# Performance work log

Measured on AMD Instinct MI355X. Metric: run time of the kernel, lower is better.

The kernel has to match this reference:

```python
import jax, jax.numpy as jnp
import numpy as np

S = 8          # num_slots
DSLOT = 128    # slot_dim
D_IN = 768     # input feature dim
ITERS = 3      # slot_att_iter
RES = 21       # 336 // 16
NGRID = RES * RES   # 441 grid positions
NTOK = 441          # tokens kept per frame (no drop here)
NFRAME = 2
F_ = 2 * NFRAME + 1  # 5 frames per clip
CLIPS = 8
B = CLIPS * F_       # 40
SIGMA = 5.0
SCALE = DSLOT ** -0.5
EPS = 1e-8


def layernorm(x, g, b):
    m = x.mean(-1, keepdims=True)
    v = ((x - m) ** 2).mean(-1, keepdims=True)
    return (x - m) * jax.lax.rsqrt(v + 1e-5) * g + b


def setup_inputs() -> dict:
    key = jax.random.key(0)
    ks = iter(jax.random.split(key, 64))
    def nrm(shape, s=0.02):
        return jax.random.normal(next(ks), shape, jnp.float32) * s
    xs = jnp.linspace(-1.0, 1.0, RES)
    ys = jnp.linspace(-1.0, 1.0, RES)
    gx, gy = jnp.meshgrid(xs, ys)  # indexing='xy' as in torch
    abs_grid = jnp.stack([gx.ravel(), gy.ravel()], axis=-1)  # [NGRID, 2]
    return {
        "inputs": jax.random.normal(next(ks), (B, NTOK, D_IN), jnp.float32),
        "token_indices": jnp.sort(jax.random.randint(next(ks), (B, NTOK), 0, NGRID), axis=-1),
        "abs_grid": abs_grid,
        "slots_init": nrm((1, S, DSLOT), 0.1),
        "S_p_init": nrm((1, S, 1, 2), 0.02),
        "S_s_init": jax.random.uniform(next(ks), (1, S, 1, 2), jnp.float32, 0.3, 0.7),
        "WQ": nrm((DSLOT, DSLOT)), "ln_g": jnp.ones((DSLOT,)), "ln_b": jnp.zeros((DSLOT,)),
        "gru_w_ih": nrm((DSLOT, 3 * DSLOT)), "gru_w_hh": nrm((DSLOT, 3 * DSLOT)),
        "gru_b_ih": jnp.zeros((3 * DSLOT,)), "gru_b_hh": jnp.zeros((3 * DSLOT,)),
        "mlp_ln_g": jnp.ones((DSLOT,)), "mlp_ln_b": jnp.zeros((DSLOT,)),
        "mlp_w1": nrm((DSLOT, 4 * DSLOT)), "mlp_b1": jnp.zeros((4 * DSLOT,)),
        "mlp_w2": nrm((4 * DSLOT, DSLOT)), "mlp_b2": jnp.zeros((DSLOT,)),
        "WK": nrm((DSLOT, DSLOT)), "WV": nrm((DSLOT, DSLOT)),
        "Wg": nrm((2, DSLOT)), "bg": jnp.zeros((DSLOT,)),
        "Wf1": nrm((DSLOT, DSLOT)), "bf1": jnp.zeros((DSLOT,)),
        "Wf2": nrm((DSLOT, DSLOT)), "bf2": jnp.zeros((DSLOT,)),
        "im_ln1_g": jnp.ones((D_IN,)), "im_ln1_b": jnp.zeros((D_IN,)),
        "im_w1": nrm((D_IN, D_IN)), "im_b1": jnp.zeros((D_IN,)),
        "im_w2": nrm((D_IN, DSLOT)), "im_b2": jnp.zeros((DSLOT,)),
        "im_ln2_g": jnp.ones((DSLOT,)), "im_ln2_b": jnp.zeros((DSLOT,)),
        "fin_w": nrm((DSLOT, DSLOT)), "fin_b": jnp.zeros((DSLOT,)),
    }


def _forward(inputs, token_indices, abs_grid, slots_init, S_p_init, S_s_init,
             WQ, ln_g, ln_b, gru_w_ih, gru_w_hh, gru_b_ih, gru_b_hh,
             mlp_ln_g, mlp_ln_b, mlp_w1, mlp_b1, mlp_w2, mlp_b2,
             WK, WV, Wg, bg, Wf1, bf1, Wf2, bf2,
             im_ln1_g, im_ln1_b, im_w1, im_b1, im_w2, im_b2, im_ln2_g, im_ln2_b,
             fin_w, fin_b):
    Bb = inputs.shape[0]
    # initial_mlp: LN -> Linear -> ReLU -> Linear -> LN
    x = layernorm(inputs, im_ln1_g, im_ln1_b)
    x = jax.nn.relu(x @ im_w1 + im_b1)
    x = x @ im_w2 + im_b2
    x = layernorm(x, im_ln2_g, im_ln2_b)          # [B, N, Dslot]
    # K/V projections of inputs are slot-independent; compute once.
    Kx = x @ WK                                    # [B, N, Dslot]
    Vx = x @ WV
    ag = abs_grid[token_indices]                   # [B, N, 2] per-batch gather
    slots = jnp.broadcast_to(slots_init, (Bb, S, DSLOT))
    S_p = jnp.broadcast_to(S_p_init, (Bb, S, 1, 2))
    S_s = jnp.broadcast_to(S_s_init, (Bb, S, 1, 2))

    def f_net(z):  # f = Linear -> ReLU -> Linear
        return jax.nn.relu(z @ Wf1 + bf1) @ Wf2 + bf2

    attn = None
    for t in range(ITERS + 1):
        slots_prev = slots
        sn = layernorm(slots, ln_g, ln_b)
        rel = (ag[:, None] - S_p) / (S_s * SIGMA)  # [B, S, N, 2]
        gr = rel @ Wg + bg                          # [B, S, N, Dslot]
        k = f_net(Kx[:, None] + gr)
        v = f_net(Vx[:, None] + gr)
        q = sn @ WQ                                 # [B, S, Dslot]
        dots = jnp.einsum('bsd,bsjd->bsj', q, k) * SCALE
        attn = jax.nn.softmax(dots, axis=1) + EPS   # softmax over slots
        attn = attn / attn.sum(-1, keepdims=True)   # renormalize over tokens
        updates = jnp.einsum('bsjd,bsj->bsd', v, attn)
        S_p = jnp.einsum('bjd,bsj->bsd', ag, attn)[:, :, None, :]
        S_s = jnp.sqrt(jnp.einsum('bsjd,bsj->bsd', (ag[:, None] - S_p) ** 2, attn))[:, :, None, :]
        if t != ITERS:
            # torch GRUCell
            xg = updates.reshape(-1, DSLOT)
            hg = slots_prev.reshape(-1, DSLOT)
            gi = xg @ gru_w_ih + gru_b_ih
            gh = hg @ gru_w_hh + gru_b_hh
            i_r, i_z, i_n = jnp.split(gi, 3, axis=-1)
            h_r, h_z, h_n = jnp.split(gh, 3, axis=-1)
            r = jax.nn.sigmoid(i_r + h_r)
            z = jax.nn.sigmoid(i_z + h_z)
            n = jnp.tanh(i_n + r * h_n)
            slots = ((1.0 - z) * n + z * hg).reshape(Bb, S, DSLOT)
            # residual pre-LN MLP (dropout is identity in eval)
            y = layernorm(slots, mlp_ln_g, mlp_ln_b)
            y = jax.nn.relu(y @ mlp_w1 + mlp_b1) @ mlp_w2 + mlp_b2
            slots = slots + y
    slots = slots @ fin_w + fin_b
    attn_out = attn.reshape(-1, F_, S, NTOK)[:, NFRAME]  # center frame
    return slots, attn_out


def reference(inputs, token_indices, abs_grid, slots_init, S_p_init, S_s_init,
              WQ, ln_g, ln_b, gru_w_ih, gru_w_hh, gru_b_ih, gru_b_hh,
              mlp_ln_g, mlp_ln_b, mlp_w1, mlp_b1, mlp_w2, mlp_b2,
              WK, WV, Wg, bg, Wf1, bf1, Wf2, bf2,
              im_ln1_g, im_ln1_b, im_w1, im_b1, im_w2, im_b2, im_ln2_g, im_ln2_b,
              fin_w, fin_b):
    return _forward(inputs, token_indices, abs_grid, slots_init, S_p_init, S_s_init,
                    WQ, ln_g, ln_b, gru_w_ih, gru_w_hh, gru_b_ih, gru_b_hh,
                    mlp_ln_g, mlp_ln_b, mlp_w1, mlp_b1, mlp_w2, mlp_b2,
                    WK, WV, Wg, bg, Wf1, bf1, Wf2, bf2,
                    im_ln1_g, im_ln1_b, im_w1, im_b1, im_w2, im_b2, im_ln2_g, im_ln2_b,
                    fin_w, fin_b)
```

## Files before the change

### kernel.cpp

```cpp
#include <hip/hip_runtime.h>
#include <cstdio>

#define NB 40
#define NS 8
#define NT 441
#define DIN 768
#define DD 128
#define NTOT (NB*NT)
#define FSCALE 0.08838834764831843f

typedef short s8v __attribute__((ext_vector_type(8)));
typedef float f4v __attribute__((ext_vector_type(4)));

__device__ inline ushort f2bf(float f){
  unsigned u = __float_as_uint(f);
  unsigned r = (u + 0x7fffu + ((u >> 16) & 1u)) >> 16;
  return (ushort)r;
}
__device__ inline float bf2f(ushort h){ return __uint_as_float(((unsigned)h) << 16); }

struct PP {
  const float *inputs; const int *tok_idx; const float *abs_grid;
  const float *slots_init, *Sp_init, *Ss_init;
  const float *WQ, *ln_g, *ln_b;
  const float *gru_w_ih, *gru_w_hh, *gru_b_ih, *gru_b_hh;
  const float *mlp_ln_g, *mlp_ln_b, *mlp_w1, *mlp_b1, *mlp_w2, *mlp_b2;
  const float *WK, *WV, *Wg, *bg, *Wf1, *bf1, *Wf2, *bf2;
  const float *im_ln1_g, *im_ln1_b, *im_w1, *im_b1, *im_w2, *im_b2, *im_ln2_g, *im_ln2_b;
  const float *fin_w, *fin_b;
  float *x, *A_K, *A_V, *ag, *WKf, *WVf, *Wg1, *c1, *Wf2T;
  float *slots, *Sp0, *Sp1, *Ss0, *Ss1, *qW, *qb, *dots, *attn;
  float *hbar_part, *Sp_part, *hbar;
  ushort *xnh, *xnl, *hh, *hl, *W1Th, *W1Tl, *W2Th, *W2Tl;
  float *out;
};

__global__ __launch_bounds__(128) void prep_weights(PP p){
  int r = blockIdx.x, d = threadIdx.x;
  float accK = 0.f, accV = 0.f;
  for (int kk = 0; kk < DD; kk++){
    float w = p.Wf1[kk*DD + d];
    accK = fmaf(p.WK[r*DD+kk], w, accK);
    accV = fmaf(p.WV[r*DD+kk], w, accV);
  }
  p.WKf[r*DD+d] = accK; p.WVf[r*DD+d] = accV;
  if (r < 2){
    float a = 0.f;
    for (int kk = 0; kk < DD; kk++) a = fmaf(p.Wg[r*DD+kk], p.Wf1[kk*DD+d], a);
    p.Wg1[r*DD+d] = a;
  }
  if (r == 2){
    float a = 0.f;
    for (int kk = 0; kk < DD; kk++) a = fmaf(p.bg[kk], p.Wf1[kk*DD+d], a);
    p.c1[d] = a + p.bf1[d];
  }
  p.Wf2T[d*DD + r] = p.Wf2[r*DD + d];
}

__global__ __launch_bounds__(256) void transpose_split(const float* __restrict__ W,
                                                       ushort* __restrict__ WTh,
                                                       ushort* __restrict__ WTl,
                                                       int K, int N){
  __shared__ float tile[64][65];
  int tid = threadIdx.x;
  int k0 = blockIdx.x * 64, n0 = blockIdx.y * 64;
  #pragma unroll
  for (int i = 0; i < 4; i++){
    int k = i*16 + (tid >> 4);
    int n4 = (tid & 15) * 4;
    float4 v = *(const float4*)(W + (long)(k0+k)*N + n0 + n4);
    tile[k][n4+0] = v.x; tile[k][n4+1] = v.y; tile[k][n4+2] = v.z; tile[k][n4+3] = v.w;
  }
  __syncthreads();
  #pragma unroll
  for (int i = 0; i < 4; i++){
    int n = i*16 + (tid >> 4);
    int k4 = (tid & 15) * 4;
    ushort4 h4, l4;
    float v0 = tile[k4+0][n], v1 = tile[k4+1][n], v2 = tile[k4+2][n], v3 = tile[k4+3][n];
    h4.x = f2bf(v0); l4.x = f2bf(v0 - bf2f(h4.x));
    h4.y = f2bf(v1); l4.y = f2bf(v1 - bf2f(h4.y));
    h4.z = f2bf(v2); l4.z = f2bf(v2 - bf2f(h4.z));
    h4.w = f2bf(v3); l4.w = f2bf(v3 - bf2f(h4.w));
    *(ushort4*)(WTh + (long)(n0+n)*K + k0 + k4) = h4;
    *(ushort4*)(WTl + (long)(n0+n)*K + k0 + k4) = l4;
  }
}

__global__ __launch_bounds__(256) void ln1_split(PP p){
  int tok = blockIdx.x*4 + (threadIdx.x >> 6);
  int l = threadIdx.x & 63;
  const float* src = p.inputs + (long)tok*DIN;
  float4 v[3];
  float s = 0.f, s2 = 0.f;
  #pragma unroll
  for (int pp = 0; pp < 3; pp++){
    v[pp] = *(const float4*)(src + pp*256 + l*4);
    s  += v[pp].x + v[pp].y + v[pp].z + v[pp].w;
    s2 += v[pp].x*v[pp].x + v[pp].y*v[pp].y + v[pp].z*v[pp].z + v[pp].w*v[pp].w;
  }
  #pragma unroll
  for (int m = 1; m < 64; m <<= 1){ s += __shfl_xor(s, m); s2 += __shfl_xor(s2, m); }
  float mean = s*(1.f/DIN), var = s2*(1.f/DIN) - mean*mean;
  float rstd = rsqrtf(var + 1e-5f);
  #pragma unroll
  for (int pp = 0; pp < 3; pp++){
    int idx = pp*256 + l*4;
    float4 g = *(const float4*)(p.im_ln1_g + idx);
    float4 b = *(const float4*)(p.im_ln1_b + idx);
    float y0 = (v[pp].x-mean)*rstd*g.x + b.x;
    float y1 = (v[pp].y-mean)*rstd*g.y + b.y;
    float y2 = (v[pp].z-mean)*rstd*g.z + b.z;
    float y3 = (v[pp].w-mean)*rstd*g.w + b.w;
    ushort4 h4, l4;
    h4.x = f2bf(y0); l4.x = f2bf(y0 - bf2f(h4.x));
    h4.y = f2bf(y1); l4.y = f2bf(y1 - bf2f(h4.y));
    h4.z = f2bf(y2); l4.z = f2bf(y2 - bf2f(h4.z));
    h4.w = f2bf(y3); l4.w = f2bf(y3 - bf2f(h4.w));
    *(ushort4*)(p.xnh + (long)tok*DIN + idx) = h4;
    *(ushort4*)(p.xnl + (long)tok*DIN + idx) = l4;
  }
}

template<int EPI>
__global__ __launch_bounds__(256) void gemm_split(
    const ushort* __restrict__ Ah, const ushort* __restrict__ Al,
    const ushort* __restrict__ Bh, const ushort* __restrict__ Bl,
    const float* __restrict__ bias,
    ushort* __restrict__ Ch, ushort* __restrict__ Cl,
    float* __restrict__ Xout, const float* __restrict__ g2, const float* __restrict__ b2,
    int M)
{
  __shared__ __align__(16) char smem[64*132*4];
  ushort* As = (ushort*)smem;
  ushort* Bs = (ushort*)(smem + 10240);
  int tid = threadIdx.x;
  int n0 = blockIdx.x * 128, m0 = blockIdx.y * 64;
  int w = tid >> 6, lane = tid & 63;
  f4v acc[4][2];
  #pragma unroll
  for (int mf = 0; mf < 4; mf++)
    #pragma unroll
    for (int nf = 0; nf < 2; nf++) acc[mf][nf] = (f4v)(0.f);

  for (int kb = 0; kb < DIN; kb += 32){
    __syncthreads();
    #pragma unroll
    for (int i = 0; i < 2; i++){
      int c = tid + i*256;
      int s = c >> 8, r = (c >> 2) & 63, kg = c & 3;
      int gr = min(m0 + r, M-1);
      const float4 va = *(const float4*)((s ? Al : Ah) + (long)gr*DIN + kb + kg*8);
      *(float4*)(As + s*2560 + r*40 + kg*8) = va;
    }
    #pragma unroll
    for (int i = 0; i < 4; i++){
      int c = tid + i*256;
      int s = c >> 9, r = (c >> 2) & 127, kg = c & 3;
      const float4 vb = *(const float4*)((s ? Bl : Bh) + (long)(n0 + r)*DIN + kb + kg*8);
      *(float4*)(Bs + s*5120 + r*40 + kg*8) = vb;
    }
    __syncthreads();
    int kg = lane >> 4, rA = lane & 15;
    s8v a0[4], a1[4], b0[2], b1[2];
    #pragma unroll
    for (int mf = 0; mf < 4; mf++){
      a0[mf] = *(const s8v*)(As +        (mf*16 + rA)*40 + kg*8);
      a1[mf] = *(const s8v*)(As + 2560 + (mf*16 + rA)*40 + kg*8);
    }
    #pragma unroll
    for (int nf = 0; nf < 2; nf++){
      int rb = w*32 + nf*16 + rA;
      b0[nf] = *(const s8v*)(Bs +        rb*40 + kg*8);
      b1[nf] = *(const s8v*)(Bs + 5120 + rb*40 + kg*8);
    }
    #pragma unroll
    for (int mf = 0; mf < 4; mf++)
      #pragma unroll
      for (int nf = 0; nf < 2; nf++){
        acc[mf][nf] = __builtin_amdgcn_mfma_f32_16x16x32_bf16(a0[mf], b0[nf], acc[mf][nf], 0, 0, 0);
        acc[mf][nf] = __builtin_amdgcn_mfma_f32_16x16x32_bf16(a0[mf], b1[nf], acc[mf][nf], 0, 0, 0);
        acc[mf][nf] = __builtin_amdgcn_mfma_f32_16x16x32_bf16(a1[mf], b0[nf], acc[mf][nf], 0, 0, 0);
      }
  }

  int rbase = (lane >> 4) * 4, cn = lane & 15;
  if (EPI == 1){
    #pragma unroll
    for (int mf = 0; mf < 4; mf++)
      #pragma unroll
      for (int nf = 0; nf < 2; nf++){
        int n = n0 + w*32 + nf*16 + cn;
        float bs = bias[n];
        #pragma unroll
        for (int r = 0; r < 4; r++){
          int m = m0 + mf*16 + rbase + r;
          if (m < M){
            float v = fmaxf(acc[mf][nf][r] + bs, 0.f);
            ushort h = f2bf(v);
            Ch[(long)m*DIN + n] = h;
            Cl[(long)m*DIN + n] = f2bf(v - bf2f(h));
          }
        }
      }
  } else {
    __syncthreads();
    float* Dl = (float*)smem;
    #pragma unroll
    for (int mf = 0; mf < 4; mf++)
      #pragma unroll
      for (int nf = 0; nf < 2; nf++){
        int n = w*32 + nf*16 + cn;
        float bs = bias[n];
        #pragma unroll
        for (int r = 0; r < 4; r++)
          Dl[(mf*16 + rbase + r)*132 + n] = acc[mf][nf][r] + bs;
      }
    __syncthreads();
    for (int rr = 0; rr < 16; rr++){
      int row = w*16 + rr;
      float e0 = Dl[row*132 + lane], e1 = Dl[row*132 + 64 + lane];
      float s = e0 + e1, s2 = e0*e0 + e1*e1;
      #pragma unroll
      for (int m2 = 1; m2 < 64; m2 <<= 1){ s += __shfl_xor(s, m2); s2 += __shfl_xor(s2, m2); }
      float mean = s*(1.f/DD), var = s2*(1.f/DD) - mean*mean;
      float rstd = rsqrtf(var + 1e-5f);
      int m = m0 + row;
      if (m < M){
        Xout[(long)m*DD + lane]      = (e0-mean)*rstd*g2[lane]      + b2[lane];
        Xout[(long)m*DD + 64 + lane] = (e1-mean)*rstd*g2[64 + lane] + b2[64 + lane];
      }
    }
  }
}

__global__ void init_state(PP p){
  int i = blockIdx.x*256 + threadIdx.x;
  if (i < NB*NS*DD) p.slots[i] = p.slots_init[i & (NS*DD-1)];
  if (i < NB*NS*2){
    p.Sp0[i] = p.Sp_init[i & (NS*2-1)];
    p.Ss0[i] = p.Ss_init[i & (NS*2-1)];
  }
}

__global__ void gather_ag(PP p){
  int i = blockIdx.x*256 + threadIdx.x;
  if (i < NTOT){
    int idx = p.tok_idx[i];
    p.ag[i*2+0] = p.abs_grid[idx*2+0];
    p.ag[i*2+1] = p.abs_grid[idx*2+1];
  }
}

__global__ __launch_bounds__(256) void k2_proj(PP p){
  __shared__ float xt[32][132];
  int tid = threadIdx.x; int g0 = blockIdx.x * 32;
  for (int f = tid; f < 32*32; f += 256){
    int tok = f >> 5, pos = (f & 31) * 4;
    int gt = g0 + tok;
    float4 v = (gt < NTOT) ? *(const float4*)(p.x + (long)gt*DD + pos)
                           : make_float4(0.f,0.f,0.f,0.f);
    *(float4*)&xt[tok][pos] = v;
  }
  __syncthreads();
  int d = tid & 127, grp = tid >> 7;
  float aK[16], aV[16];
  float c1v = p.c1[d];
  #pragma unroll
  for (int t = 0; t < 16; t++){ aK[t] = c1v; aV[t] = c1v; }
  for (int kk = 0; kk < DD; kk += 4){
    float k0 = p.WKf[(kk+0)*DD+d], k1 = p.WKf[(kk+1)*DD+d], k2 = p.WKf[(kk+2)*DD+d], k3 = p.WKf[(kk+3)*DD+d];
    float v0 = p.WVf[(kk+0)*DD+d], v1 = p.WVf[(kk+1)*DD+d], v2 = p.WVf[(kk+2)*DD+d], v3 = p.WVf[(kk+3)*DD+d];
    #pragma unroll
    for (int t = 0; t < 16; t++){
      float4 xv = *(const float4*)&xt[grp*16+t][kk];
      aK[t] = fmaf(xv.x,k0, fmaf(xv.y,k1, fmaf(xv.z,k2, fmaf(xv.w,k3, aK[t]))));
      aV[t] = fmaf(xv.x,v0, fmaf(xv.y,v1, fmaf(xv.z,v2, fmaf(xv.w,v3, aV[t]))));
    }
  }
  #pragma unroll
  for (int t = 0; t < 16; t++){
    int gt = g0 + grp*16 + t;
    if (gt < NTOT){ p.A_K[(long)gt*DD+d] = aK[t]; p.A_V[(long)gt*DD+d] = aV[t]; }
  }
}

__global__ __launch_bounds__(128) void k3_slots(PP p){
  int bs = blockIdx.x, d = threadIdx.x;
  __shared__ float sn[128], q[128];
  __shared__ float rs[2][2];
  float v = p.slots[bs*DD+d];
  float s = v, s2 = v*v;
  for (int m = 1; m < 64; m <<= 1){ s += __shfl_xor(s, m); s2 += __shfl_xor(s2, m); }
  if ((d & 63) == 0){ rs[d>>6][0] = s; rs[d>>6][1] = s2; }
  __syncthreads();
  s = rs[0][0] + rs[1][0]; s2 = rs[0][1] + rs[1][1];
  float mean = s*(1.f/DD), var = s2*(1.f/DD) - mean*mean, rstd = rsqrtf(var + 1e-5f);
  sn[d] = (v-mean)*rstd*p.ln_g[d] + p.ln_b[d];
  __syncthreads();
  float acc = 0.f;
  for (int kk = 0; kk < DD; kk++) acc = fmaf(sn[kk], p.WQ[kk*DD+d], acc);
  q[d] = acc;
  __syncthreads();
  float a2 = 0.f;
  for (int dd = 0; dd < DD; dd++) a2 = fmaf(q[dd], p.Wf2T[dd*DD+d], a2);
  p.qW[bs*DD+d] = a2;
  float pb = p.bf2[d]*q[d];
  for (int m = 1; m < 64; m <<= 1) pb += __shfl_xor(pb, m);
  if ((d & 63) == 0) rs[d>>6][0] = pb;
  __syncthreads();
  if (d == 0) p.qb[bs] = (rs[0][0] + rs[1][0]) * FSCALE;
}

__global__ __launch_bounds__(256) void k4_dots(PP p, const float* Sp, const float* Ss){
  int b = blockIdx.x / 7, tile = blockIdx.x % 7;
  int tid = threadIdx.x, wid = tid >> 6, lane = tid & 63;
  int tl = lane >> 2, dg = lane & 3;
  __shared__ float qws[8][132];
  __shared__ float spss[8][4];
  __shared__ float qbs[8];
  for (int f = tid; f < 8*128; f += 256){
    int s = f >> 7, d = f & 127;
    qws[s][(d&31)*4 + (d>>5)] = p.qW[(b*NS+s)*DD+d];
  }
  if (tid < 8) qbs[tid] = p.qb[b*NS+tid];
  if (tid < 32){
    int s = tid >> 2, c = tid & 3;
    spss[s][c] = (c < 2) ? Sp[(b*NS+s)*2+c] : 1.f/(Ss[(b*NS+s)*2+(c-2)]*5.0f);
  }
  __syncthreads();
  int j = tile*64 + wid*16 + tl;
  bool valid = j < NT;
  int jj = valid ? j : 0;
  float aa[32], w0[32], w1[32];
  {
    const float* src = p.A_K + ((long)(b*NT+jj))*DD + dg*32;
    #pragma unroll
    for (int i4 = 0; i4 < 8; i4++){
      float4 t = *(const float4*)(src + i4*4);
      aa[i4*4+0]=t.x; aa[i4*4+1]=t.y; aa[i4*4+2]=t.z; aa[i4*4+3]=t.w;
    }
    #pragma unroll
    for (int i4 = 0; i4 < 8; i4++){
      float4 t0 = *(const float4*)(p.Wg1 + dg*32 + i4*4);
      float4 t1 = *(const float4*)(p.Wg1 + DD + dg*32 + i4*4);
      w0[i4*4+0]=t0.x; w0[i4*4+1]=t0.y; w0[i4*4+2]=t0.z; w0[i4*4+3]=t0.w;
      w1[i4*4+0]=t1.x; w1[i4*4+1]=t1.y; w1[i4*4+2]=t1.z; w1[i4*4+3]=t1.w;
    }
  }
  float ag0 = p.ag[(b*NT+jj)*2], ag1 = p.ag[(b*NT+jj)*2+1];
  #pragma unroll
  for (int s = 0; s < 8; s++){
    float rel0 = (ag0 - spss[s][0])*spss[s][2];
    float rel1 = (ag1 - spss[s][1])*spss[s][3];
    float acc = 0.f;
    #pragma unroll
    for (int i = 0; i < 32; i++){
      float hk = fmaxf(fmaf(rel0, w0[i], fmaf(rel1, w1[i], aa[i])), 0.f);
      acc = fmaf(hk, qws[s][i*4+dg], acc);
    }
    acc += __shfl_xor(acc, 1); acc += __shfl_xor(acc, 2);
    if (dg == 0 && valid) p.dots[(b*NS+s)*NT + j] = acc*FSCALE + qbs[s];
  }
}

__global__ __launch_bounds__(256) void k5_softmax(PP p){
  int b = blockIdx.x, tid = threadIdx.x;
  float a0[8], a1[8];
  float psum[8];
  #pragma unroll
  for (int s = 0; s < 8; s++) psum[s] = 0.f;
  bool has1 = (tid + 256) < NT;
  {
    int j = tid;
    float dv[8]; float m = -1e30f;
    #pragma unroll
    for (int s = 0; s < 8; s++){ dv[s] = p.dots[(b*NS+s)*NT+j]; m = fmaxf(m, dv[s]); }
    float tot = 0.f;
    #pragma unroll
    for (int s = 0; s < 8; s++){ dv[s] = expf(dv[s]-m); tot += dv[s]; }
    float inv = 1.f/tot;
    #pragma unroll
    for (int s = 0; s < 8; s++){ a0[s] = dv[s]*inv + 1e-8f; psum[s] += a0[s]; }
  }
  if (has1){
    int j = tid + 256;
    float dv[8]; float m = -1e30f;
    #pragma unroll
    for (int s = 0; s < 8; s++){ dv[s] = p.dots[(b*NS+s)*NT+j]; m = fmaxf(m, dv[s]); }
    float tot = 0.f;
    #pragma unroll
    for (int s = 0; s < 8; s++){ dv[s] = expf(dv[s]-m); tot += dv[s]; }
    float inv = 1.f/tot;
    #pragma unroll
    for (int s = 0; s < 8; s++){ a1[s] = dv[s]*inv + 1e-8f; psum[s] += a1[s]; }
  }
  #pragma unroll
  for (int s = 0; s < 8; s++)
    for (int m2 = 1; m2 < 64; m2 <<= 1) psum[s] += __shfl_xor(psum[s], m2);
  __shared__ float wsum[4][8];
  __shared__ float sums[8];
  if ((tid & 63) == 0)
    for (int s = 0; s < 8; s++) wsum[tid>>6][s] = psum[s];
  __syncthreads();
  if (tid < 8) sums[tid] = wsum[0][tid]+wsum[1][tid]+wsum[2][tid]+wsum[3][tid];
  __syncthreads();
  {
    int j = tid;
    #pragma unroll
    for (int s = 0; s < 8; s++) p.attn[(b*NS+s)*NT+j] = a0[s]/sums[s];
  }
  if (has1){
    int j = tid + 256;
    #pragma unroll
    for (int s = 0; s < 8; s++) p.attn[(b*NS+s)*NT+j] = a1[s]/sums[s];
  }
}

__global__ __launch_bounds__(256) void k6a(PP p, const float* Sp, const float* Ss){
  int b = blockIdx.x >> 3, tile = blockIdx.x & 7;
  int tid = threadIdx.x, wid = tid >> 6, lane = tid & 63;
  int j0 = tile*56; int jn = min(NT, j0+56) - j0;
  __shared__ float atile[8][56];
  __shared__ float spss[8][4];
  __shared__ float hpart[4][8][128];
  __shared__ float ppart[4][8][2];
  for (int f = tid; f < 8*56; f += 256){
    int s = f/56, jj = f%56;
    atile[s][jj] = (j0+jj < NT) ? p.attn[(b*NS+s)*NT + j0+jj] : 0.f;
  }
  if (tid < 32){
    int s = tid >> 2, c = tid & 3;
    spss[s][c] = (c < 2) ? Sp[(b*NS+s)*2+c] : 1.f/(Ss[(b*NS+s)*2+(c-2)]*5.0f);
  }
  __syncthreads();
  int d0 = lane, d1 = lane + 64;
  float wg00 = p.Wg1[d0], wg10 = p.Wg1[DD+d0], wg01 = p.Wg1[d1], wg11 = p.Wg1[DD+d1];
  float acc0[8], acc1[8], accp[8];
  #pragma unroll
  for (int s = 0; s < 8; s++){ acc0[s]=0.f; acc1[s]=0.f; accp[s]=0.f; }
  int cpar = lane & 1;
  for (int jj = wid; jj < jn; jj += 4){
    int j = j0 + jj;
    float av0 = p.A_V[((long)(b*NT+j))*DD + d0];
    float av1 = p.A_V[((long)(b*NT+j))*DD + d1];
    float ag0 = p.ag[(b*NT+j)*2], ag1 = p.ag[(b*NT+j)*2+1];
    float agc = cpar ? ag1 : ag0;
    #pragma unroll
    for (int s = 0; s < 8; s++){
      float rel0 = (ag0 - spss[s][0])*spss[s][2];
      float rel1 = (ag1 - spss[s][1])*spss[s][3];
      float a = atile[s][jj];
      float hv0 = fmaxf(fmaf(rel0,wg00, fmaf(rel1,wg10, av0)), 0.f);
      float hv1 = fmaxf(fmaf(rel0,wg01, fmaf(rel1,wg11, av1)), 0.f);
      acc0[s] = fmaf(a, hv0, acc0[s]);
      acc1[s] = fmaf(a, hv1, acc1[s]);
      if (lane < 2) accp[s] = fmaf(a, agc, accp[s]);
    }
  }
  #pragma unroll
  for (int s = 0; s < 8; s++){ hpart[wid][s][d0] = acc0[s]; hpart[wid][s][d1] = acc1[s]; }
  if (lane < 2)
    for (int s = 0; s < 8; s++) ppart[wid][s][lane] = accp[s];
  __syncthreads();
  for (int f = tid; f < 8*128; f += 256){
    int s = f >> 7, d = f & 127;
    p.hbar_part[((b*8+tile)*NS+s)*DD+d] = hpart[0][s][d]+hpart[1][s][d]+hpart[2][s][d]+hpart[3][s][d];
  }
  if (tid < 16){
    int s = tid >> 1, c = tid & 1;
    p.Sp_part[((b*8+tile)*NS+s)*2+c] = ppart[0][s][c]+ppart[1][s][c]+ppart[2][s][c]+ppart[3][s][c];
  }
}

__global__ __launch_bounds__(128) void k6r(PP p, float* Sp_new, float* Ss_new){
  int bs = blockIdx.x; int b = bs >> 3, s = bs & 7, d = threadIdx.x;
  float v = 0.f;
  for (int t = 0; t < 8; t++) v += p.hbar_part[((b*8+t)*NS+s)*DD+d];
  p.hbar[bs*DD+d] = v;
  __shared__ float spl[2];
  if (d < 2){
    float u = 0.f;
    for (int t = 0; t < 8; t++) u += p.Sp_part[((b*8+t)*NS+s)*2+d];
    Sp_new[bs*2+d] = u; spl[d] = u;
  }
  __syncthreads();
  float sp0 = spl[0], sp1 = spl[1];
  float q0 = 0.f, q1 = 0.f;
  for (int j = d; j < NT; j += 128){
    float at = p.attn[bs*NT+j];
    float e0 = p.ag[(b*NT+j)*2]   - sp0;
    float e1 = p.ag[(b*NT+j)*2+1] - sp1;
    q0 = fmaf(at, e0*e0, q0); q1 = fmaf(at, e1*e1, q1);
  }
  for (int m = 1; m < 64; m <<= 1){ q0 += __shfl_xor(q0, m); q1 += __shfl_xor(q1, m); }
  __shared__ float rr[2][2];
  if ((d & 63) == 0){ rr[d>>6][0] = q0; rr[d>>6][1] = q1; }
  __syncthreads();
  if (d == 0){
    Ss_new[bs*2+0] = sqrtf(rr[0][0]+rr[1][0]);
    Ss_new[bs*2+1] = sqrtf(rr[0][1]+rr[1][1]);
  }
}

__global__ __launch_bounds__(128) void k7_update(PP p){
  int bs = blockIdx.x, d = threadIdx.x;
  __shared__ float hb[128], upd[128], hprev[128], y[128], h1[512];
  __shared__ float rr[2][2];
  hb[d] = p.hbar[bs*DD+d]; hprev[d] = p.slots[bs*DD+d];
  __syncthreads();
  float a = p.bf2[d];
  for (int kk = 0; kk < DD; kk++) a = fmaf(hb[kk], p.Wf2[kk*DD+d], a);
  upd[d] = a;
  __syncthreads();
  float gi[3], gh[3];
  #pragma unroll
  for (int i = 0; i < 3; i++){ gi[i] = p.gru_b_ih[d+128*i]; gh[i] = p.gru_b_hh[d+128*i]; }
  for (int kk = 0; kk < DD; kk++){
    float xv = upd[kk], hv = hprev[kk];
    #pragma unroll
    for (int i = 0; i < 3; i++){
      gi[i] = fmaf(xv, p.gru_w_ih[kk*384 + d+128*i], gi[i]);
      gh[i] = fmaf(hv, p.gru_w_hh[kk*384 + d+128*i], gh[i]);
    }
  }
  float r = 1.f/(1.f+expf(-(gi[0]+gh[0])));
  float z = 1.f/(1.f+expf(-(gi[1]+gh[1])));
  float n = tanhf(gi[2] + r*gh[2]);
  float hnew = (1.f-z)*n + z*hprev[d];
  float s = hnew, s2 = hnew*hnew;
  for (int m = 1; m < 64; m <<= 1){ s += __shfl_xor(s, m); s2 += __shfl_xor(s2, m); }
  if ((d & 63) == 0){ rr[d>>6][0] = s; rr[d>>6][1] = s2; }
  __syncthreads();
  s = rr[0][0]+rr[1][0]; s2 = rr[0][1]+rr[1][1];
  float mean = s*(1.f/DD), var = s2*(1.f/DD)-mean*mean, rstd = rsqrtf(var+1e-5f);
  y[d] = (hnew-mean)*rstd*p.mlp_ln_g[d] + p.mlp_ln_b[d];
  __syncthreads();
  #pragma unroll
  for (int i = 0; i < 4; i++){
    int o = d + 128*i;
    float acc = p.mlp_b1[o];
    for (int kk = 0; kk < DD; kk++) acc = fmaf(y[kk], p.mlp_w1[kk*512+o], acc);
    h1[o] = fmaxf(acc, 0.f);
  }
  __syncthreads();
  float acc2 = p.mlp_b2[d];
  for (int o = 0; o < 512; o++) acc2 = fmaf(h1[o], p.mlp_w2[o*DD+d], acc2);
  p.slots[bs*DD+d] = hnew + acc2;
}

__global__ __launch_bounds__(128) void k8_final(PP p){
  int bs = blockIdx.x, d = threadIdx.x;
  __shared__ float sl[128];
  sl[d] = p.slots[bs*DD+d];
  __syncthreads();
  float a = p.fin_b[d];
  for (int kk = 0; kk < DD; kk++) a = fmaf(sl[kk], p.fin_w[kk*DD+d], a);
  p.out[bs*DD+d] = a;
}

__global__ void k8_attn(PP p){
  int i = blockIdx.x*256 + threadIdx.x;
  if (i < 8*NS*NT){
    int clip = i / (NS*NT);
    int rem  = i % (NS*NT);
    int b = clip*5 + 2;
    p.out[NB*NS*DD + i] = p.attn[b*NS*NT + rem];
  }
}

extern "C" void kernel_launch(void* const* d_in, const int* in_sizes, int n_in,
                              void* d_out, int out_size, void* d_ws, size_t ws_size,
                              hipStream_t stream){
  PP p;
  p.inputs=(const float*)d_in[0]; p.tok_idx=(const int*)d_in[1]; p.abs_grid=(const float*)d_in[2];
  p.slots_init=(const float*)d_in[3]; p.Sp_init=(const float*)d_in[4]; p.Ss_init=(const float*)d_in[5];
  p.WQ=(const float*)d_in[6]; p.ln_g=(const float*)d_in[7]; p.ln_b=(const float*)d_in[8];
  p.gru_w_ih=(const float*)d_in[9]; p.gru_w_hh=(const float*)d_in[10];
  p.gru_b_ih=(const float*)d_in[11]; p.gru_b_hh=(const float*)d_in[12];
  p.mlp_ln_g=(const float*)d_in[13]; p.mlp_ln_b=(const float*)d_in[14];
  p.mlp_w1=(const float*)d_in[15]; p.mlp_b1=(const float*)d_in[16];
  p.mlp_w2=(const float*)d_in[17]; p.mlp_b2=(const float*)d_in[18];
  p.WK=(const float*)d_in[19]; p.WV=(const float*)d_in[20]; p.Wg=(const float*)d_in[21]; p.bg=(const float*)d_in[22];
  p.Wf1=(const float*)d_in[23]; p.bf1=(const float*)d_in[24]; p.Wf2=(const float*)d_in[25]; p.bf2=(const float*)d_in[26];
  p.im_ln1_g=(const float*)d_in[27]; p.im_ln1_b=(const float*)d_in[28];
  p.im_w1=(const float*)d_in[29]; p.im_b1=(const float*)d_in[30];
  p.im_w2=(const float*)d_in[31]; p.im_b2=(const float*)d_in[32];
  p.im_ln2_g=(const float*)d_in[33]; p.im_ln2_b=(const float*)d_in[34];
  p.fin_w=(const float*)d_in[35]; p.fin_b=(const float*)d_in[36];

  float* w = (float*)d_ws;
  size_t need = 0;
  auto alloc = [&](size_t nfl){ nfl = (nfl + 3) & ~(size_t)3; float* r = w + need; need += nfl; return r; };
  p.x    = alloc((size_t)NTOT*DD);
  p.A_K  = alloc((size_t)NTOT*DD);
  p.A_V  = alloc((size_t)NTOT*DD);
  p.ag   = alloc((size_t)NTOT*2);
  p.WKf  = alloc(DD*DD);
  p.WVf  = alloc(DD*DD);
  p.Wg1  = alloc(2*DD);
  p.c1   = alloc(DD);
  p.Wf2T = alloc(DD*DD);
  p.slots= alloc(NB*NS*DD);
  p.Sp0  = alloc(NB*NS*2);
  p.Sp1  = alloc(NB*NS*2);
  p.Ss0  = alloc(NB*NS*2);
  p.Ss1  = alloc(NB*NS*2);
  p.qW   = alloc(NB*NS*DD);
  p.qb   = alloc(NB*NS);
  p.dots = alloc((size_t)NB*NS*NT);
  p.attn = alloc((size_t)NB*NS*NT);
  p.hbar_part = alloc((size_t)NB*8*NS*DD);
  p.Sp_part   = alloc((size_t)NB*8*NS*2);
  p.hbar = alloc(NB*NS*DD);
  p.xnh  = (ushort*)alloc((size_t)NTOT*DIN/2);
  p.xnl  = (ushort*)alloc((size_t)NTOT*DIN/2);
  p.hh   = (ushort*)alloc((size_t)NTOT*DIN/2);
  p.hl   = (ushort*)alloc((size_t)NTOT*DIN/2);
  p.W1Th = (ushort*)alloc((size_t)DIN*DIN/2);
  p.W1Tl = (ushort*)alloc((size_t)DIN*DIN/2);
  p.W2Th = (ushort*)alloc((size_t)DD*DIN/2);
  p.W2Tl = (ushort*)alloc((size_t)DD*DIN/2);
  p.out = (float*)d_out;
  if (ws_size < need*sizeof(float)){
    fprintf(stderr, "kernel_launch: ws too small (%zu < %zu)\n", ws_size, need*sizeof(float));
    return;
  }

  prep_weights<<<dim3(DD), dim3(DD), 0, stream>>>(p);
  transpose_split<<<dim3(DIN/64, DIN/64), dim3(256), 0, stream>>>(p.im_w1, p.W1Th, p.W1Tl, DIN, DIN);
  transpose_split<<<dim3(DIN/64, DD/64), dim3(256), 0, stream>>>(p.im_w2, p.W2Th, p.W2Tl, DIN, DD);
  init_state<<<dim3((NB*NS*DD+255)/256), dim3(256), 0, stream>>>(p);
  gather_ag<<<dim3((NTOT+255)/256), dim3(256), 0, stream>>>(p);
  ln1_split<<<dim3(NTOT/4), dim3(256), 0, stream>>>(p);
  gemm_split<1><<<dim3(DIN/128, (NTOT+63)/64), dim3(256), 0, stream>>>(
      p.xnh, p.xnl, p.W1Th, p.W1Tl, p.im_b1, p.hh, p.hl,
      nullptr, nullptr, nullptr, NTOT);
  gemm_split<2><<<dim3(1, (NTOT+63)/64), dim3(256), 0, stream>>>(
      p.hh, p.hl, p.W2Th, p.W2Tl, p.im_b2, nullptr, nullptr,
      p.x, p.im_ln2_g, p.im_ln2_b, NTOT);
  k2_proj<<<dim3((NTOT+31)/32), dim3(256), 0, stream>>>(p);

  float* Sp[2] = {p.Sp0, p.Sp1};
  float* Ss[2] = {p.Ss0, p.Ss1};
  int cur = 0;
  for (int t = 0; t < 4; t++){
    k3_slots<<<dim3(NB*NS), dim3(128), 0, stream>>>(p);
    k4_dots<<<dim3(NB*7), dim3(256), 0, stream>>>(p, Sp[cur], Ss[cur]);
    k5_softmax<<<dim3(NB), dim3(256), 0, stream>>>(p);
    if (t < 3){
      k6a<<<dim3(NB*8), dim3(256), 0, stream>>>(p, Sp[cur], Ss[cur]);
      k6r<<<dim3(NB*NS), dim3(128), 0, stream>>>(p, Sp[cur^1], Ss[cur^1]);
      k7_update<<<dim3(NB*NS), dim3(128), 0, stream>>>(p);
      cur ^= 1;
    }
  }
  k8_final<<<dim3(NB*NS), dim3(128), 0, stream>>>(p);
  k8_attn<<<dim3((8*NS*NT+255)/256), dim3(256), 0, stream>>>(p);
}
```

Measured before the change: 477.3 us.

## Fuse slot-attention iteration loop into one persistent kernel with grid barriers

Replaces the per-iteration chain of small kernels (slot projection, dots, softmax, weighted sums, reductions, GRU/MLP update, final projection and attention output) with a single persistent kernel of 320 blocks, one per batch-slot pair. Phases are separated by a global atomic barrier. Slot state and position/scale stay in shared memory, and the softmax is folded into the dots phase. The goal is to remove about 25 kernel launches and their global round trips. The risk is that the spin barrier deadlocks if not all 320 blocks are co-resident, and each block now does the per-slot reductions over all tokens serially.

New measurement: 1.393 ms. 192% more time.

```diff
diff --git a/kernel.cpp b/kernel.cpp
--- a/kernel.cpp
+++ b/kernel.cpp
@@ -7,6 +7,7 @@
 #define DIN 768
 #define DD 128
 #define NTOT (NB*NT)
+#define NBLK 320
 #define FSCALE 0.08838834764831843f
 
 typedef short s8v __attribute__((ext_vector_type(8)));
@@ -28,15 +29,27 @@
   const float *WK, *WV, *Wg, *bg, *Wf1, *bf1, *Wf2, *bf2;
   const float *im_ln1_g, *im_ln1_b, *im_w1, *im_b1, *im_w2, *im_b2, *im_ln2_g, *im_ln2_b;
   const float *fin_w, *fin_b;
-  float *x, *A_K, *A_V, *ag, *WKf, *WVf, *Wg1, *c1, *Wf2T;
-  float *slots, *Sp0, *Sp1, *Ss0, *Ss1, *qW, *qb, *dots, *attn;
-  float *hbar_part, *Sp_part, *hbar;
+  float *x, *A_K, *A_V, *WKf, *WVf, *Wg1, *c1, *Wf2T;
+  float *qw_g, *qb_g, *spss_g, *a_g, *ag_g;
+  int *bar;
   ushort *xnh, *xnl, *hh, *hl, *W1Th, *W1Tl, *W2Th, *W2Tl;
   float *out;
 };
 
+__device__ inline void gsync(int* bar, int idx, int nblk){
+  __syncthreads();
+  if (threadIdx.x == 0){
+    __threadfence();
+    atomicAdd(&bar[idx], 1);
+    while (__hip_atomic_load(&bar[idx], __ATOMIC_ACQUIRE, __HIP_MEMORY_SCOPE_AGENT) < nblk)
+      __builtin_amdgcn_s_sleep(1);
+  }
+  __syncthreads();
+}
+
 __global__ __launch_bounds__(128) void prep_weights(PP p){
   int r = blockIdx.x, d = threadIdx.x;
+  if (r == 0 && d < 16) p.bar[d] = 0;
   float accK = 0.f, accV = 0.f;
   for (int kk = 0; kk < DD; kk++){
     float w = p.Wf1[kk*DD + d];
@@ -131,9 +144,9 @@
     float* __restrict__ Xout, const float* __restrict__ g2, const float* __restrict__ b2,
     int M)
 {
-  __shared__ __align__(16) char smem[64*132*4];
-  ushort* As = (ushort*)smem;
-  ushort* Bs = (ushort*)(smem + 10240);
+  __shared__ __align__(16) char smemc[64*132*4];
+  ushort* As = (ushort*)smemc;
+  ushort* Bs = (ushort*)(smemc + 10240);
   int tid = threadIdx.x;
   int n0 = blockIdx.x * 128, m0 = blockIdx.y * 64;
   int w = tid >> 6, lane = tid & 63;
@@ -205,7 +218,7 @@
       }
   } else {
     __syncthreads();
-    float* Dl = (float*)smem;
+    float* Dl = (float*)smemc;
     #pragma unroll
     for (int mf = 0; mf < 4; mf++)
       #pragma unroll
@@ -234,24 +247,6 @@
   }
 }
 
-__global__ void init_state(PP p){
-  int i = blockIdx.x*256 + threadIdx.x;
-  if (i < NB*NS*DD) p.slots[i] = p.slots_init[i & (NS*DD-1)];
-  if (i < NB*NS*2){
-    p.Sp0[i] = p.Sp_init[i & (NS*2-1)];
-    p.Ss0[i] = p.Ss_init[i & (NS*2-1)];
-  }
-}
-
-__global__ void gather_ag(PP p){
-  int i = blockIdx.x*256 + threadIdx.x;
-  if (i < NTOT){
-    int idx = p.tok_idx[i];
-    p.ag[i*2+0] = p.abs_grid[idx*2+0];
-    p.ag[i*2+1] = p.abs_grid[idx*2+1];
-  }
-}
-
 __global__ __launch_bounds__(256) void k2_proj(PP p){
   __shared__ float xt[32][132];
   int tid = threadIdx.x; int g0 = blockIdx.x * 32;
@@ -285,287 +280,281 @@
   }
 }
 
-__global__ __launch_bounds__(128) void k3_slots(PP p){
-  int bs = blockIdx.x, d = threadIdx.x;
-  __shared__ float sn[128], q[128];
-  __shared__ float rs[2][2];
-  float v = p.slots[bs*DD+d];
-  float s = v, s2 = v*v;
-  for (int m = 1; m < 64; m <<= 1){ s += __shfl_xor(s, m); s2 += __shfl_xor(s2, m); }
-  if ((d & 63) == 0){ rs[d>>6][0] = s; rs[d>>6][1] = s2; }
-  __syncthreads();
-  s = rs[0][0] + rs[1][0]; s2 = rs[0][1] + rs[1][1];
-  float mean = s*(1.f/DD), var = s2*(1.f/DD) - mean*mean, rstd = rsqrtf(var + 1e-5f);
-  sn[d] = (v-mean)*rstd*p.ln_g[d] + p.ln_b[d];
+__device__ void phase0(const PP& p, int bs, int tid, float* sm, const float* slrow, const float* spst){
+  float* sn   = sm;
+  float* qv   = sm + 128;
+  float* part = sm + 256;
+  float* red  = sm + 512;
+  int o = tid & 127, h = tid >> 7;
+  float v = (tid < 128) ? slrow[tid] : 0.f;
+  float s1 = v, s2 = v*v;
+  #pragma unroll
+  for (int m = 1; m < 64; m <<= 1){ s1 += __shfl_xor(s1, m); s2 += __shfl_xor(s2, m); }
+  if (tid < 128 && (tid & 63) == 0){ red[(tid>>6)*2] = s1; red[(tid>>6)*2+1] = s2; }
+  __syncthreads();
+  float mean = (red[0]+red[2])*(1.f/128.f);
+  float var  = (red[1]+red[3])*(1.f/128.f) - mean*mean;
+  float rstd = rsqrtf(var + 1e-5f);
+  if (tid < 128) sn[tid] = (v-mean)*rstd*p.ln_g[tid] + p.ln_b[tid];
   __syncthreads();
   float acc = 0.f;
-  for (int kk = 0; kk < DD; kk++) acc = fmaf(sn[kk], p.WQ[kk*DD+d], acc);
-  q[d] = acc;
-  __syncthreads();
-  float a2 = 0.f;
-  for (int dd = 0; dd < DD; dd++) a2 = fmaf(q[dd], p.Wf2T[dd*DD+d], a2);
-  p.qW[bs*DD+d] = a2;
-  float pb = p.bf2[d]*q[d];
+  for (int k = 0; k < 64; k++) acc = fmaf(sn[h*64+k], p.WQ[(h*64+k)*128+o], acc);
+  part[h*128+o] = acc;
+  __syncthreads();
+  if (tid < 128) qv[tid] = part[tid] + part[128+tid];
+  __syncthreads();
+  float acc2 = 0.f;
+  for (int k = 0; k < 64; k++) acc2 = fmaf(qv[h*64+k], p.Wf2T[(h*64+k)*128+o], acc2);
+  part[h*128+o] = acc2;
+  __syncthreads();
+  if (tid < 128) p.qw_g[(long)bs*128+tid] = part[tid] + part[128+tid];
+  float pb = (tid < 128) ? qv[tid]*p.bf2[tid] : 0.f;
+  #pragma unroll
   for (int m = 1; m < 64; m <<= 1) pb += __shfl_xor(pb, m);
-  if ((d & 63) == 0) rs[d>>6][0] = pb;
-  __syncthreads();
-  if (d == 0) p.qb[bs] = (rs[0][0] + rs[1][0]) * FSCALE;
-}
-
-__global__ __launch_bounds__(256) void k4_dots(PP p, const float* Sp, const float* Ss){
-  int b = blockIdx.x / 7, tile = blockIdx.x % 7;
-  int tid = threadIdx.x, wid = tid >> 6, lane = tid & 63;
-  int tl = lane >> 2, dg = lane & 3;
-  __shared__ float qws[8][132];
-  __shared__ float spss[8][4];
-  __shared__ float qbs[8];
-  for (int f = tid; f < 8*128; f += 256){
-    int s = f >> 7, d = f & 127;
-    qws[s][(d&31)*4 + (d>>5)] = p.qW[(b*NS+s)*DD+d];
-  }
-  if (tid < 8) qbs[tid] = p.qb[b*NS+tid];
-  if (tid < 32){
-    int s = tid >> 2, c = tid & 3;
-    spss[s][c] = (c < 2) ? Sp[(b*NS+s)*2+c] : 1.f/(Ss[(b*NS+s)*2+(c-2)]*5.0f);
-  }
-  __syncthreads();
-  int j = tile*64 + wid*16 + tl;
-  bool valid = j < NT;
-  int jj = valid ? j : 0;
-  float aa[32], w0[32], w1[32];
+  if ((tid & 63) == 0) red[4 + (tid>>6)] = pb;
+  __syncthreads();
+  if (tid == 0){
+    p.qb_g[bs] = FSCALE*(red[4]+red[5]+red[6]+red[7]);
+    p.spss_g[bs*4+0] = spst[0]; p.spss_g[bs*4+1] = spst[1];
+    p.spss_g[bs*4+2] = 1.f/(spst[2]*5.0f); p.spss_g[bs*4+3] = 1.f/(spst[3]*5.0f);
+  }
+  __syncthreads();
+}
+
+__global__ __launch_bounds__(256, 2) void k_pers(PP p){
+  __shared__ float smem[4608];
+  const int blk = blockIdx.x, tid = threadIdx.x;
+  const int bs = blk, bb = blk >> 3, ss = blk & 7;
+  float* sl   = smem + 4352;
+  float* spst = smem + 4480;
+  int bi = 0;
+
+  if (tid < 128) sl[tid] = p.slots_init[ss*128+tid];
+  if (tid < 4)   spst[tid] = (tid < 2) ? p.Sp_init[ss*2+tid] : p.Ss_init[ss*2+(tid-2)];
+  if (ss == 0){
+    for (int f = tid; f < 448; f += 256){
+      float g0 = 0.f, g1 = 0.f;
+      if (f < NT){ int idx = p.tok_idx[bb*NT+f]; g0 = p.abs_grid[idx*2]; g1 = p.abs_grid[idx*2+1]; }
+      p.ag_g[((long)bb*448+f)*2]   = g0;
+      p.ag_g[((long)bb*448+f)*2+1] = g1;
+    }
+  }
+  __syncthreads();
+  phase0(p, bs, tid, smem, sl, spst);
+  gsync(p.bar, bi++, NBLK);
+
+  for (int t = 0; t < 4; t++){
+    {
+      float* qws = smem;
+      float* wg  = smem + 1024;
+      float* qbs = smem + 1280;
+      float* spl = smem + 1288;
+      for (int f = tid; f < 1024; f += 256){
+        int s = f >> 7, d = f & 127;
+        qws[s*128 + (d&15)*8 + (d>>4)] = p.qw_g[((long)bb*8+s)*128 + d];
+      }
+      wg[tid] = p.Wg1[tid];
+      if (tid < 8)  qbs[tid] = p.qb_g[bb*8+tid];
+      if (tid < 32) spl[tid] = p.spss_g[bb*32+tid];
+      __syncthreads();
+      int dg = tid & 7;
+      float w0[16], w1[16];
+      #pragma unroll
+      for (int i = 0; i < 16; i++){ w0[i] = wg[dg*16+i]; w1[i] = wg[128+dg*16+i]; }
+      #pragma unroll
+      for (int pass = 0; pass < 2; pass++){
+        int jj = pass*32 + (tid >> 3);
+        int j = ss*56 + jj;
+        bool valid = (jj < 56) && (j < NT);
+        int jcl = valid ? j : 0;
+        float aa[16];
+        const float* src = p.A_K + ((long)(bb*NT+jcl))*DD + dg*16;
+        #pragma unroll
+        for (int i4 = 0; i4 < 4; i4++){
+          float4 tt = *(const float4*)(src + i4*4);
+          aa[i4*4]=tt.x; aa[i4*4+1]=tt.y; aa[i4*4+2]=tt.z; aa[i4*4+3]=tt.w;
+        }
+        float g0 = p.ag_g[((long)bb*448+jcl)*2], g1 = p.ag_g[((long)bb*448+jcl)*2+1];
+        float dv[8];
+        #pragma unroll
+        for (int s = 0; s < 8; s++){
+          float rel0 = (g0 - spl[s*4])*spl[s*4+2];
+          float rel1 = (g1 - spl[s*4+1])*spl[s*4+3];
+          float acc = 0.f;
+          #pragma unroll
+          for (int i = 0; i < 16; i++){
+            float hk = fmaxf(fmaf(rel0, w0[i], fmaf(rel1, w1[i], aa[i])), 0.f);
+            acc = fmaf(hk, qws[s*128 + i*8 + dg], acc);
+          }
+          acc += __shfl_xor(acc, 1); acc += __shfl_xor(acc, 2); acc += __shfl_xor(acc, 4);
+          dv[s] = acc*FSCALE + qbs[s];
+        }
+        if (dg == 0 && valid){
+          float m = -1e30f;
+          #pragma unroll
+          for (int s = 0; s < 8; s++) m = fmaxf(m, dv[s]);
+          float tot = 0.f;
+          #pragma unroll
+          for (int s = 0; s < 8; s++){ dv[s] = expf(dv[s]-m); tot += dv[s]; }
+          float inv = 1.f/tot;
+          #pragma unroll
+          for (int s = 0; s < 8; s++) p.a_g[((long)(bb*8+s))*448 + j] = dv[s]*inv + 1e-8f;
+        }
+      }
+    }
+    gsync(p.bar, bi++, NBLK);
+
+    {
+      float* a_l = smem;
+      float* agx = smem + 448;
+      float* agy = smem + 896;
+      float* red = smem + 1344;
+      float* bc  = smem + 1360;
+      float* spl = smem + 1376;
+      for (int f = tid; f < 448; f += 256){
+        bool v = f < NT;
+        a_l[f] = v ? p.a_g[(long)bs*448+f] : 0.f;
+        agx[f] = v ? p.ag_g[((long)bb*448+f)*2]   : 0.f;
+        agy[f] = v ? p.ag_g[((long)bb*448+f)*2+1] : 0.f;
+      }
+      if (tid < 4) spl[tid] = p.spss_g[bs*4+tid];
+      __syncthreads();
+      float sa = 0.f, s0 = 0.f, s1 = 0.f;
+      for (int jx = tid; jx < 448; jx += 256){
+        float a = a_l[jx];
+        sa += a; s0 = fmaf(a, agx[jx], s0); s1 = fmaf(a, agy[jx], s1);
+      }
+      #pragma unroll
+      for (int m = 1; m < 64; m <<= 1){ sa += __shfl_xor(sa,m); s0 += __shfl_xor(s0,m); s1 += __shfl_xor(s1,m); }
+      if ((tid & 63) == 0){ int w = tid>>6; red[w*4]=sa; red[w*4+1]=s0; red[w*4+2]=s1; }
+      __syncthreads();
+      if (tid == 0){
+        float SA = red[0]+red[4]+red[8]+red[12];
+        float S0 = red[1]+red[5]+red[9]+red[13];
+        float S1 = red[2]+red[6]+red[10]+red[14];
+        bc[0] = S0/SA; bc[1] = S1/SA; bc[2] = 1.f/SA;
+      }
+      __syncthreads();
+      if (t == 3){
+        if ((bb % 5) == 2){
+          float inv = bc[2];
+          long base = (long)NB*NS*DD + (long)(bb/5)*(NS*NT) + (long)ss*NT;
+          for (int jx = tid; jx < NT; jx += 256) p.out[base+jx] = a_l[jx]*inv;
+        }
+      } else {
+        float Sp0 = bc[0], Sp1 = bc[1];
+        float q0 = 0.f, q1 = 0.f;
+        for (int jx = tid; jx < 448; jx += 256){
+          float a = a_l[jx];
+          float e0 = agx[jx]-Sp0, e1 = agy[jx]-Sp1;
+          q0 = fmaf(a, e0*e0, q0); q1 = fmaf(a, e1*e1, q1);
+        }
+        #pragma unroll
+        for (int m = 1; m < 64; m <<= 1){ q0 += __shfl_xor(q0,m); q1 += __shfl_xor(q1,m); }
+        if ((tid & 63) == 0){ int w = tid>>6; red[w*4]=q0; red[w*4+1]=q1; }
+        __syncthreads();
+        if (tid == 0){
+          float Q0 = red[0]+red[4]+red[8]+red[12];
+          float Q1 = red[1]+red[5]+red[9]+red[13];
+          spst[0] = Sp0; spst[1] = Sp1;
+          spst[2] = sqrtf(Q0*bc[2]); spst[3] = sqrtf(Q1*bc[2]);
+        }
+        __syncthreads();
+        int d = tid & 127, jp = tid >> 7;
+        float sp0 = spl[0], sp1 = spl[1], si0 = spl[2], si1 = spl[3];
+        float wgd0 = p.Wg1[d], wgd1 = p.Wg1[DD+d];
+        float acc = 0.f;
+        for (int j = jp; j < NT; j += 2){
+          float av = p.A_V[((long)(bb*NT+j))*DD + d];
+          float rel0 = (agx[j]-sp0)*si0, rel1 = (agy[j]-sp1)*si1;
+          float hv = fmaxf(fmaf(rel0, wgd0, fmaf(rel1, wgd1, av)), 0.f);
+          acc = fmaf(a_l[j], hv, acc);
+        }
+        float* hpart = smem + 1536;
+        float* hb    = smem + 1792;
+        hpart[jp*128+d] = acc;
+        __syncthreads();
+        if (tid < 128) hb[tid] = (hpart[tid] + hpart[128+tid]) * bc[2];
+        __syncthreads();
+        float* part = smem + 1920;
+        int o = tid & 127, h = tid >> 7;
+        float acc2 = 0.f;
+        for (int k = 0; k < 64; k++) acc2 = fmaf(hb[h*64+k], p.Wf2[(h*64+k)*128+o], acc2);
+        part[h*128+o] = acc2;
+        __syncthreads();
+        float* upd = smem + 2176;
+        if (tid < 128) upd[tid] = part[tid] + part[128+tid] + p.bf2[tid];
+        __syncthreads();
+        float* gil = smem + 2432;
+        float* ghl = smem + 2816;
+        int oA = tid, oB = tid + 256;
+        float giA = p.gru_b_ih[oA], ghA = p.gru_b_hh[oA];
+        float giB = 0.f, ghB = 0.f;
+        if (tid < 128){ giB = p.gru_b_ih[oB]; ghB = p.gru_b_hh[oB]; }
+        for (int k = 0; k < 128; k++){
+          float uk = upd[k], sk = sl[k];
+          giA = fmaf(uk, p.gru_w_ih[k*384+oA], giA);
+          ghA = fmaf(sk, p.gru_w_hh[k*384+oA], ghA);
+          if (tid < 128){
+            giB = fmaf(uk, p.gru_w_ih[k*384+oB], giB);
+            ghB = fmaf(sk, p.gru_w_hh[k*384+oB], ghB);
+          }
+        }
+        gil[oA] = giA; ghl[oA] = ghA;
+        if (tid < 128){ gil[oB] = giB; ghl[oB] = ghB; }
+        __syncthreads();
+        float* hnl = smem + 1408;
+        float hnv = 0.f;
+        if (tid < 128){
+          float r = 1.f/(1.f+expf(-(gil[tid]+ghl[tid])));
+          float z = 1.f/(1.f+expf(-(gil[128+tid]+ghl[128+tid])));
+          float n = tanhf(gil[256+tid] + r*ghl[256+tid]);
+          hnv = (1.f-z)*n + z*sl[tid];
+        }
+        float t1 = hnv, t2 = hnv*hnv;
+        #pragma unroll
+        for (int m = 1; m < 64; m <<= 1){ t1 += __shfl_xor(t1,m); t2 += __shfl_xor(t2,m); }
+        if (tid < 128 && (tid & 63) == 0){ red[(tid>>6)*2] = t1; red[(tid>>6)*2+1] = t2; }
+        __syncthreads();
+        float mean = (red[0]+red[2])*(1.f/128.f);
+        float var  = (red[1]+red[3])*(1.f/128.f) - mean*mean;
+        float rstd = rsqrtf(var + 1e-5f);
+        float* yv = smem + 3200;
+        if (tid < 128){
+          hnl[tid] = hnv;
+          yv[tid] = (hnv-mean)*rstd*p.mlp_ln_g[tid] + p.mlp_ln_b[tid];
+        }
+        __syncthreads();
+        float* h1 = smem + 3328;
+        float m1A = p.mlp_b1[tid], m1B = p.mlp_b1[tid+256];
+        for (int k = 0; k < 128; k++){
+          float y = yv[k];
+          m1A = fmaf(y, p.mlp_w1[k*512+tid], m1A);
+          m1B = fmaf(y, p.mlp_w1[k*512+tid+256], m1B);
+        }
+        h1[tid] = fmaxf(m1A, 0.f); h1[tid+256] = fmaxf(m1B, 0.f);
+        __syncthreads();
+        float a2 = 0.f;
+        for (int kk = 0; kk < 256; kk++) a2 = fmaf(h1[h*256+kk], p.mlp_w2[(h*256+kk)*128+o], a2);
+        part[h*128+o] = a2;
+        __syncthreads();
+        if (tid < 128) sl[tid] = hnl[tid] + p.mlp_b2[tid] + part[tid] + part[128+tid];
+        __syncthreads();
+        phase0(p, bs, tid, smem, sl, spst);
+      }
+    }
+    if (t < 3) gsync(p.bar, bi++, NBLK);
+  }
+
   {
-    const float* src = p.A_K + ((long)(b*NT+jj))*DD + dg*32;
-    #pragma unroll
-    for (int i4 = 0; i4 < 8; i4++){
-      float4 t = *(const float4*)(src + i4*4);
-      aa[i4*4+0]=t.x; aa[i4*4+1]=t.y; aa[i4*4+2]=t.z; aa[i4*4+3]=t.w;
-    }
-    #pragma unroll
-    for (int i4 = 0; i4 < 8; i4++){
-      float4 t0 = *(const float4*)(p.Wg1 + dg*32 + i4*4);
-      float4 t1 = *(const float4*)(p.Wg1 + DD + dg*32 + i4*4);
-      w0[i4*4+0]=t0.x; w0[i4*4+1]=t0.y; w0[i4*4+2]=t0.z; w0[i4*4+3]=t0.w;
-      w1[i4*4+0]=t1.x; w1[i4*4+1]=t1.y; w1[i4*4+2]=t1.z; w1[i4*4+3]=t1.w;
-    }
-  }
-  float ag0 = p.ag[(b*NT+jj)*2], ag1 = p.ag[(b*NT+jj)*2+1];
-  #pragma unroll
-  for (int s = 0; s < 8; s++){
-    float rel0 = (ag0 - spss[s][0])*spss[s][2];
-    float rel1 = (ag1 - spss[s][1])*spss[s][3];
+    __syncthreads();
+    float* part = smem + 256;
+    int o = tid & 127, h = tid >> 7;
     float acc = 0.f;
-    #pragma unroll
-    for (int i = 0; i < 32; i++){
-      float hk = fmaxf(fmaf(rel0, w0[i], fmaf(rel1, w1[i], aa[i])), 0.f);
-      acc = fmaf(hk, qws[s][i*4+dg], acc);
-    }
-    acc += __shfl_xor(acc, 1); acc += __shfl_xor(acc, 2);
-    if (dg == 0 && valid) p.dots[(b*NS+s)*NT + j] = acc*FSCALE + qbs[s];
-  }
-}
-
-__global__ __launch_bounds__(256) void k5_softmax(PP p){
-  int b = blockIdx.x, tid = threadIdx.x;
-  float a0[8], a1[8];
-  float psum[8];
-  #pragma unroll
-  for (int s = 0; s < 8; s++) psum[s] = 0.f;
-  bool has1 = (tid + 256) < NT;
-  {
-    int j = tid;
-    float dv[8]; float m = -1e30f;
-    #pragma unroll
-    for (int s = 0; s < 8; s++){ dv[s] = p.dots[(b*NS+s)*NT+j]; m = fmaxf(m, dv[s]); }
-    float tot = 0.f;
-    #pragma unroll
-    for (int s = 0; s < 8; s++){ dv[s] = expf(dv[s]-m); tot += dv[s]; }
-    float inv = 1.f/tot;
-    #pragma unroll
-    for (int s = 0; s < 8; s++){ a0[s] = dv[s]*inv + 1e-8f; psum[s] += a0[s]; }
-  }
-  if (has1){
-    int j = tid + 256;
-    float dv[8]; float m = -1e30f;
-    #pragma unroll
-    for (int s = 0; s < 8; s++){ dv[s] = p.dots[(b*NS+s)*NT+j]; m = fmaxf(m, dv[s]); }
-    float tot = 0.f;
-    #pragma unroll
-    for (int s = 0; s < 8; s++){ dv[s] = expf(dv[s]-m); tot += dv[s]; }
-    float inv = 1.f/tot;
-    #pragma unroll
-    for (int s = 0; s < 8; s++){ a1[s] = dv[s]*inv + 1e-8f; psum[s] += a1[s]; }
-  }
-  #pragma unroll
-  for (int s = 0; s < 8; s++)
-    for (int m2 = 1; m2 < 64; m2 <<= 1) psum[s] += __shfl_xor(psum[s], m2);
-  __shared__ float wsum[4][8];
-  __shared__ float sums[8];
-  if ((tid & 63) == 0)
-    for (int s = 0; s < 8; s++) wsum[tid>>6][s] = psum[s];
-  __syncthreads();
-  if (tid < 8) sums[tid] = wsum[0][tid]+wsum[1][tid]+wsum[2][tid]+wsum[3][tid];
-  __syncthreads();
-  {
-    int j = tid;
-    #pragma unroll
-    for (int s = 0; s < 8; s++) p.attn[(b*NS+s)*NT+j] = a0[s]/sums[s];
-  }
-  if (has1){
-    int j = tid + 256;
-    #pragma unroll
-    for (int s = 0; s < 8; s++) p.attn[(b*NS+s)*NT+j] = a1[s]/sums[s];
-  }
-}
-
-__global__ __launch_bounds__(256) void k6a(PP p, const float* Sp, const float* Ss){
-  int b = blockIdx.x >> 3, tile = blockIdx.x & 7;
-  int tid = threadIdx.x, wid = tid >> 6, lane = tid & 63;
-  int j0 = tile*56; int jn = min(NT, j0+56) - j0;
-  __shared__ float atile[8][56];
-  __shared__ float spss[8][4];
-  __shared__ float hpart[4][8][128];
-  __shared__ float ppart[4][8][2];
-  for (int f = tid; f < 8*56; f += 256){
-    int s = f/56, jj = f%56;
-    atile[s][jj] = (j0+jj < NT) ? p.attn[(b*NS+s)*NT + j0+jj] : 0.f;
-  }
-  if (tid < 32){
-    int s = tid >> 2, c = tid & 3;
-    spss[s][c] = (c < 2) ? Sp[(b*NS+s)*2+c] : 1.f/(Ss[(b*NS+s)*2+(c-2)]*5.0f);
-  }
-  __syncthreads();
-  int d0 = lane, d1 = lane + 64;
-  float wg00 = p.Wg1[d0], wg10 = p.Wg1[DD+d0], wg01 = p.Wg1[d1], wg11 = p.Wg1[DD+d1];
-  float acc0[8], acc1[8], accp[8];
-  #pragma unroll
-  for (int s = 0; s < 8; s++){ acc0[s]=0.f; acc1[s]=0.f; accp[s]=0.f; }
-  int cpar = lane & 1;
-  for (int jj = wid; jj < jn; jj += 4){
-    int j = j0 + jj;
-    float av0 = p.A_V[((long)(b*NT+j))*DD + d0];
-    float av1 = p.A_V[((long)(b*NT+j))*DD + d1];
-    float ag0 = p.ag[(b*NT+j)*2], ag1 = p.ag[(b*NT+j)*2+1];
-    float agc = cpar ? ag1 : ag0;
-    #pragma unroll
-    for (int s = 0; s < 8; s++){
-      float rel0 = (ag0 - spss[s][0])*spss[s][2];
-      float rel1 = (ag1 - spss[s][1])*spss[s][3];
-      float a = atile[s][jj];
-      float hv0 = fmaxf(fmaf(rel0,wg00, fmaf(rel1,wg10, av0)), 0.f);
-      float hv1 = fmaxf(fmaf(rel0,wg01, fmaf(rel1,wg11, av1)), 0.f);
-      acc0[s] = fmaf(a, hv0, acc0[s]);
-      acc1[s] = fmaf(a, hv1, acc1[s]);
-      if (lane < 2) accp[s] = fmaf(a, agc, accp[s]);
-    }
-  }
-  #pragma unroll
-  for (int s = 0; s < 8; s++){ hpart[wid][s][d0] = acc0[s]; hpart[wid][s][d1] = acc1[s]; }
-  if (lane < 2)
-    for (int s = 0; s < 8; s++) ppart[wid][s][lane] = accp[s];
-  __syncthreads();
-  for (int f = tid; f < 8*128; f += 256){
-    int s = f >> 7, d = f & 127;
-    p.hbar_part[((b*8+tile)*NS+s)*DD+d] = hpart[0][s][d]+hpart[1][s][d]+hpart[2][s][d]+hpart[3][s][d];
-  }
-  if (tid < 16){
-    int s = tid >> 1, c = tid & 1;
-    p.Sp_part[((b*8+tile)*NS+s)*2+c] = ppart[0][s][c]+ppart[1][s][c]+ppart[2][s][c]+ppart[3][s][c];
-  }
-}
-
-__global__ __launch_bounds__(128) void k6r(PP p, float* Sp_new, float* Ss_new){
-  int bs = blockIdx.x; int b = bs >> 3, s = bs & 7, d = threadIdx.x;
-  float v = 0.f;
-  for (int t = 0; t < 8; t++) v += p.hbar_part[((b*8+t)*NS+s)*DD+d];
-  p.hbar[bs*DD+d] = v;
-  __shared__ float spl[2];
-  if (d < 2){
-    float u = 0.f;
-    for (int t = 0; t < 8; t++) u += p.Sp_part[((b*8+t)*NS+s)*2+d];
-    Sp_new[bs*2+d] = u; spl[d] = u;
-  }
-  __syncthreads();
-  float sp0 = spl[0], sp1 = spl[1];
-  float q0 = 0.f, q1 = 0.f;
-  for (int j = d; j < NT; j += 128){
-    float at = p.attn[bs*NT+j];
-    float e0 = p.ag[(b*NT+j)*2]   - sp0;
-    float e1 = p.ag[(b*NT+j)*2+1] - sp1;
-    q0 = fmaf(at, e0*e0, q0); q1 = fmaf(at, e1*e1, q1);
-  }
-  for (int m = 1; m < 64; m <<= 1){ q0 += __shfl_xor(q0, m); q1 += __shfl_xor(q1, m); }
-  __shared__ float rr[2][2];
-  if ((d & 63) == 0){ rr[d>>6][0] = q0; rr[d>>6][1] = q1; }
-  __syncthreads();
-  if (d == 0){
-    Ss_new[bs*2+0] = sqrtf(rr[0][0]+rr[1][0]);
-    Ss_new[bs*2+1] = sqrtf(rr[0][1]+rr[1][1]);
-  }
-}
-
-__global__ __launch_bounds__(128) void k7_update(PP p){
-  int bs = blockIdx.x, d = threadIdx.x;
-  __shared__ float hb[128], upd[128], hprev[128], y[128], h1[512];
-  __shared__ float rr[2][2];
-  hb[d] = p.hbar[bs*DD+d]; hprev[d] = p.slots[bs*DD+d];
-  __syncthreads();
-  float a = p.bf2[d];
-  for (int kk = 0; kk < DD; kk++) a = fmaf(hb[kk], p.Wf2[kk*DD+d], a);
-  upd[d] = a;
-  __syncthreads();
-  float gi[3], gh[3];
-  #pragma unroll
-  for (int i = 0; i < 3; i++){ gi[i] = p.gru_b_ih[d+128*i]; gh[i] = p.gru_b_hh[d+128*i]; }
-  for (int kk = 0; kk < DD; kk++){
-    float xv = upd[kk], hv = hprev[kk];
-    #pragma unroll
-    for (int i = 0; i < 3; i++){
-      gi[i] = fmaf(xv, p.gru_w_ih[kk*384 + d+128*i], gi[i]);
-      gh[i] = fmaf(hv, p.gru_w_hh[kk*384 + d+128*i], gh[i]);
-    }
-  }
-  float r = 1.f/(1.f+expf(-(gi[0]+gh[0])));
-  float z = 1.f/(1.f+expf(-(gi[1]+gh[1])));
-  float n = tanhf(gi[2] + r*gh[2]);
-  float hnew = (1.f-z)*n + z*hprev[d];
-  float s = hnew, s2 = hnew*hnew;
-  for (int m = 1; m < 64; m <<= 1){ s += __shfl_xor(s, m); s2 += __shfl_xor(s2, m); }
-  if ((d & 63) == 0){ rr[d>>6][0] = s; rr[d>>6][1] = s2; }
-  __syncthreads();
-  s = rr[0][0]+rr[1][0]; s2 = rr[0][1]+rr[1][1];
-  float mean = s*(1.f/DD), var = s2*(1.f/DD)-mean*mean, rstd = rsqrtf(var+1e-5f);
-  y[d] = (hnew-mean)*rstd*p.mlp_ln_g[d] + p.mlp_ln_b[d];
-  __syncthreads();
-  #pragma unroll
-  for (int i = 0; i < 4; i++){
-    int o = d + 128*i;
-    float acc = p.mlp_b1[o];
-    for (int kk = 0; kk < DD; kk++) acc = fmaf(y[kk], p.mlp_w1[kk*512+o], acc);
-    h1[o] = fmaxf(acc, 0.f);
-  }
-  __syncthreads();
-  float acc2 = p.mlp_b2[d];
-  for (int o = 0; o < 512; o++) acc2 = fmaf(h1[o], p.mlp_w2[o*DD+d], acc2);
-  p.slots[bs*DD+d] = hnew + acc2;
-}
-
-__global__ __launch_bounds__(128) void k8_final(PP p){
-  int bs = blockIdx.x, d = threadIdx.x;
-  __shared__ float sl[128];
-  sl[d] = p.slots[bs*DD+d];
-  __syncthreads();
-  float a = p.fin_b[d];
-  for (int kk = 0; kk < DD; kk++) a = fmaf(sl[kk], p.fin_w[kk*DD+d], a);
-  p.out[bs*DD+d] = a;
-}
-
-__global__ void k8_attn(PP p){
-  int i = blockIdx.x*256 + threadIdx.x;
-  if (i < 8*NS*NT){
-    int clip = i / (NS*NT);
-    int rem  = i % (NS*NT);
-    int b = clip*5 + 2;
-    p.out[NB*NS*DD + i] = p.attn[b*NS*NT + rem];
+    for (int k = 0; k < 64; k++) acc = fmaf(sl[h*64+k], p.fin_w[(h*64+k)*128+o], acc);
+    part[h*128+o] = acc;
+    __syncthreads();
+    if (tid < 128) p.out[(long)bs*128+tid] = p.fin_b[tid] + part[tid] + part[128+tid];
   }
 }
 
@@ -595,24 +584,17 @@
   p.x    = alloc((size_t)NTOT*DD);
   p.A_K  = alloc((size_t)NTOT*DD);
   p.A_V  = alloc((size_t)NTOT*DD);
-  p.ag   = alloc((size_t)NTOT*2);
   p.WKf  = alloc(DD*DD);
   p.WVf  = alloc(DD*DD);
   p.Wg1  = alloc(2*DD);
   p.c1   = alloc(DD);
   p.Wf2T = alloc(DD*DD);
-  p.slots= alloc(NB*NS*DD);
-  p.Sp0  = alloc(NB*NS*2);
-  p.Sp1  = alloc(NB*NS*2);
-  p.Ss0  = alloc(NB*NS*2);
-  p.Ss1  = alloc(NB*NS*2);
-  p.qW   = alloc(NB*NS*DD);
-  p.qb   = alloc(NB*NS);
-  p.dots = alloc((size_t)NB*NS*NT);
-  p.attn = alloc((size_t)NB*NS*NT);
-  p.hbar_part = alloc((size_t)NB*8*NS*DD);
-  p.Sp_part   = alloc((size_t)NB*8*NS*2);
-  p.hbar = alloc(NB*NS*DD);
+  p.qw_g   = alloc(320*128);
+  p.qb_g   = alloc(320);
+  p.spss_g = alloc(320*4);
+  p.a_g    = alloc((size_t)320*448);
+  p.ag_g   = alloc((size_t)40*448*2);
+  p.bar    = (int*)alloc(16);
   p.xnh  = (ushort*)alloc((size_t)NTOT*DIN/2);
   p.xnl  = (ushort*)alloc((size_t)NTOT*DIN/2);
   p.hh   = (ushort*)alloc((size_t)NTOT*DIN/2);
@@ -627,11 +609,9 @@
     return;
   }
 
-  prep_weights<<<dim3(DD), dim3(DD), 0, stream>>>(p);
+  prep_weights<<<dim3(DD), dim3(128), 0, stream>>>(p);
   transpose_split<<<dim3(DIN/64, DIN/64), dim3(256), 0, stream>>>(p.im_w1, p.W1Th, p.W1Tl, DIN, DIN);
   transpose_split<<<dim3(DIN/64, DD/64), dim3(256), 0, stream>>>(p.im_w2, p.W2Th, p.W2Tl, DIN, DD);
-  init_state<<<dim3((NB*NS*DD+255)/256), dim3(256), 0, stream>>>(p);
-  gather_ag<<<dim3((NTOT+255)/256), dim3(256), 0, stream>>>(p);
   ln1_split<<<dim3(NTOT/4), dim3(256), 0, stream>>>(p);
   gemm_split<1><<<dim3(DIN/128, (NTOT+63)/64), dim3(256), 0, stream>>>(
       p.xnh, p.xnl, p.W1Th, p.W1Tl, p.im_b1, p.hh, p.hl,
@@ -640,21 +620,5 @@
       p.hh, p.hl, p.W2Th, p.W2Tl, p.im_b2, nullptr, nullptr,
       p.x, p.im_ln2_g, p.im_ln2_b, NTOT);
   k2_proj<<<dim3((NTOT+31)/32), dim3(256), 0, stream>>>(p);
-
-  float* Sp[2] = {p.Sp0, p.Sp1};
-  float* Ss[2] = {p.Ss0, p.Ss1};
-  int cur = 0;
-  for (int t = 0; t < 4; t++){
-    k3_slots<<<dim3(NB*NS), dim3(128), 0, stream>>>(p);
-    k4_dots<<<dim3(NB*7), dim3(256), 0, stream>>>(p, Sp[cur], Ss[cur]);
-    k5_softmax<<<dim3(NB), dim3(256), 0, stream>>>(p);
-    if (t < 3){
-      k6a<<<dim3(NB*8), dim3(256), 0, stream>>>(p, Sp[cur], Ss[cur]);
-      k6r<<<dim3(NB*NS), dim3(128), 0, stream>>>(p, Sp[cur^1], Ss[cur^1]);
-      k7_update<<<dim3(NB*NS), dim3(128), 0, stream>>>(p);
-      cur ^= 1;
-    }
-  }
-  k8_final<<<dim3(NB*NS), dim3(128), 0, stream>>>(p);
-  k8_attn<<<dim3((8*NS*NT+255)/256), dim3(256), 0, stream>>>(p);
-}
+  k_pers<<<dim3(NBLK), dim3(256), 0, stream>>>(p);
+}
```
